# Kernel tuning notes

Measured on AMD Instinct MI355X. Metric: run time of the kernel, lower is better.

The kernel has to match this reference:

```python
import jax, jax.numpy as jnp
import numpy as np

EPS = 1e-5

def _layernorm(x, g, b):
    mu = jnp.mean(x, axis=-1, keepdims=True)
    var = jnp.mean(jnp.square(x - mu), axis=-1, keepdims=True)
    return (x - mu) * jax.lax.rsqrt(var + EPS) * g + b

def setup_inputs() -> dict:
    key = jax.random.key(0)
    ks = jax.random.split(key, 5)
    F_, H, D = 1024, 16, 64
    B, N = 4, 2048
    s = lambda k, shp, fan: jax.random.normal(k, shp, jnp.float32) * (fan ** -0.5)
    return {
        "x": jax.random.normal(ks[0], (B, N, F_), jnp.float32),
        "Wq": s(ks[1], (H * D, F_), F_),
        "Wkv": s(ks[2], (2 * H * D, F_), F_),
        "Wo": s(ks[3], (F_, H * D), H * D),
        "ln_g": jnp.ones((F_,), jnp.float32),
        "ln_b": jnp.zeros((F_,), jnp.float32),
        "lnc_g": jnp.ones((F_,), jnp.float32),
        "lnc_b": jnp.zeros((F_,), jnp.float32),
    }

def reference(x, Wq, Wkv, Wo, ln_g, ln_b, lnc_g, lnc_b):
    H, D = 16, 64
    scale = D ** -0.5
    skip = x
    xn = _layernorm(x, ln_g, ln_b)          # query path norm
    cn = _layernorm(x, lnc_g, lnc_b)        # context (self) norm
    B, N, _ = x.shape
    q = jnp.einsum('bnf,ef->bne', xn, Wq)   # [B,N,H*D]
    kv = jnp.einsum('bnf,ef->bne', cn, Wkv) # [B,N,2*H*D]
    k, v = jnp.split(kv, 2, axis=-1)
    tohd = lambda t: t.reshape(B, N, H, D).transpose(0, 2, 1, 3)  # b h n d
    q, k, v = tohd(q), tohd(k), tohd(v)
    sim = jnp.einsum('bhnd,bhmd->bhnm', q, k) * scale
    attn = jax.nn.softmax(sim, axis=-1)
    out = jnp.einsum('bhnm,bhmd->bhnd', attn, v)
    out = out.transpose(0, 2, 1, 3).reshape(B, N, H * D)
    out = jnp.einsum('bne,fe->bnf', out, Wo)
    return skip + out
```

## Files before the change

kernel.cpp:

```cpp
#include <hip/hip_runtime.h>
#include <hip/hip_bf16.h>
#include <stdint.h>

typedef __bf16 bf16;
typedef __bf16 bf16x8 __attribute__((ext_vector_type(8)));
typedef __bf16 bf16x4 __attribute__((ext_vector_type(4)));
typedef float f32x4 __attribute__((ext_vector_type(4)));
typedef unsigned u32x2 __attribute__((ext_vector_type(2)));

#define F_DIM 1024
#define NSEQ  2048
#define NB    4
#define NH    16
#define HD    64
#define MROWS (NB * NSEQ)
#define LOG2E 1.44269504088896340736f

__device__ __forceinline__ void gload_lds16(const void* g, void* l) {
    __builtin_amdgcn_global_load_lds(
        (__attribute__((address_space(1))) void*)g,
        (__attribute__((address_space(3))) void*)l,
        16, 0, 0);
}

__device__ __forceinline__ unsigned lds_addr(const void* p) {
    return (unsigned)(size_t)(__attribute__((address_space(3))) const void*)p;
}

__device__ __forceinline__ float exp2_fast(float x) {
    float r;
    asm("v_exp_f32 %0, %1" : "=v"(r) : "v"(x));
    return r;
}

__device__ __forceinline__ unsigned cvtpk_bf16(float lo, float hi) {
    unsigned r;
    asm("v_cvt_pk_bf16_f32 %0, %1, %2" : "=v"(r) : "v"(lo), "v"(hi));
    return r;
}

__global__ __launch_bounds__(256) void prep_kernel(
    const float* __restrict__ x,
    const float* __restrict__ g1, const float* __restrict__ b1,
    const float* __restrict__ g2, const float* __restrict__ b2,
    bf16* __restrict__ xn, bf16* __restrict__ cn,
    const float* __restrict__ wq, const float* __restrict__ wkv,
    const float* __restrict__ wo, bf16* __restrict__ wdst)
{
    const int t = threadIdx.x;
    if (blockIdx.x >= MROWS) {
        const int i = (blockIdx.x - MROWS) * 256 + t;
        const float* src;
        int si;
        if (i < 262144)       { src = wq;  si = i; }
        else if (i < 786432)  { src = wkv; si = i - 262144; }
        else                  { src = wo;  si = i - 786432; }
        float4 v = reinterpret_cast<const float4*>(src)[si];
        bf16x4 o = { (bf16)v.x, (bf16)v.y, (bf16)v.z, (bf16)v.w };
        reinterpret_cast<bf16x4*>(wdst)[i] = o;
        return;
    }
    const int row = blockIdx.x;
    float4 v = reinterpret_cast<const float4*>(x + (size_t)row * F_DIM)[t];
    float s  = v.x + v.y + v.z + v.w;
    float ss = v.x * v.x + v.y * v.y + v.z * v.z + v.w * v.w;
#pragma unroll
    for (int m = 1; m < 64; m <<= 1) {
        s  += __shfl_xor(s, m);
        ss += __shfl_xor(ss, m);
    }
    __shared__ float red[8];
    const int w = t >> 6;
    if ((t & 63) == 0) { red[w] = s; red[4 + w] = ss; }
    __syncthreads();
    s  = red[0] + red[1] + red[2] + red[3];
    ss = red[4] + red[5] + red[6] + red[7];
    const float mu  = s * (1.0f / F_DIM);
    const float var = fmaxf(ss * (1.0f / F_DIM) - mu * mu, 0.0f);
    const float rs  = rsqrtf(var + 1e-5f);

    float4 G1 = reinterpret_cast<const float4*>(g1)[t];
    float4 B1 = reinterpret_cast<const float4*>(b1)[t];
    float4 G2 = reinterpret_cast<const float4*>(g2)[t];
    float4 B2 = reinterpret_cast<const float4*>(b2)[t];
    const float h0 = (v.x - mu) * rs, h1 = (v.y - mu) * rs;
    const float h2 = (v.z - mu) * rs, h3 = (v.w - mu) * rs;
    bf16x4 o1 = { (bf16)(h0 * G1.x + B1.x), (bf16)(h1 * G1.y + B1.y),
                  (bf16)(h2 * G1.z + B1.z), (bf16)(h3 * G1.w + B1.w) };
    bf16x4 o2 = { (bf16)(h0 * G2.x + B2.x), (bf16)(h1 * G2.y + B2.y),
                  (bf16)(h2 * G2.z + B2.z), (bf16)(h3 * G2.w + B2.w) };
    *reinterpret_cast<bf16x4*>(xn + (size_t)row * F_DIM + t * 4) = o1;
    *reinterpret_cast<bf16x4*>(cn + (size_t)row * F_DIM + t * 4) = o2;
}

__global__ __launch_bounds__(256, 2) void qkv_gemm(
    const bf16* __restrict__ xn, const bf16* __restrict__ cn,
    const bf16* __restrict__ wq, const bf16* __restrict__ wkv,
    bf16* __restrict__ qb, bf16* __restrict__ kvb, float qscale)
{
    __shared__ bf16 As[128 * 32];
    __shared__ bf16 Bs[128 * 32];
    const int t = threadIdx.x;
    const int lane = t & 63;
    const int w = t >> 6;
    const int wr = w >> 1, wc = w & 1;

    int flat = blockIdx.x;
    flat = (flat & 7) * 192 + (flat >> 3);

    const bf16 *A, *B;
    bf16* C;
    int N, bm, bn;
    float osc;
    if (flat < 512) {
        A = xn; B = wq; C = qb; N = 1024; osc = qscale;
        bm = (flat >> 3) * 128; bn = (flat & 7) * 128;
    } else {
        const int f = flat - 512;
        A = cn; B = wkv; C = kvb; N = 2048; osc = 1.0f;
        bm = (f >> 4) * 128; bn = (f & 15) * 128;
    }

    const int r = lane & 15;
    const int kg = (lane >> 4) * 8;

    f32x4 acc[4][4];
#pragma unroll
    for (int i = 0; i < 4; i++)
#pragma unroll
        for (int j = 0; j < 4; j++) acc[i][j] = (f32x4){0.f, 0.f, 0.f, 0.f};

    const int c0 = t, c1 = 256 + t;
    const size_t aoff0 = (size_t)(bm + (c0 >> 2)) * F_DIM + (c0 & 3) * 8;
    const size_t aoff1 = (size_t)(bm + (c1 >> 2)) * F_DIM + (c1 & 3) * 8;
    const size_t boff0 = (size_t)(bn + (c0 >> 2)) * F_DIM + (c0 & 3) * 8;
    const size_t boff1 = (size_t)(bn + (c1 >> 2)) * F_DIM + (c1 & 3) * 8;
    bf16* lA0 = As + (size_t)(0 * 256 + w * 64) * 8;
    bf16* lA1 = As + (size_t)(1 * 256 + w * 64) * 8;
    bf16* lB0 = Bs + (size_t)(0 * 256 + w * 64) * 8;
    bf16* lB1 = Bs + (size_t)(1 * 256 + w * 64) * 8;

    for (int kt = 0; kt < F_DIM; kt += 32) {
        gload_lds16(A + aoff0 + kt, lA0);
        gload_lds16(A + aoff1 + kt, lA1);
        gload_lds16(B + boff0 + kt, lB0);
        gload_lds16(B + boff1 + kt, lB1);
        __syncthreads();
        bf16x8 af[4], bfr[4];
#pragma unroll
        for (int mi = 0; mi < 4; mi++)
            af[mi] = *(const bf16x8*)(As + (wr * 64 + mi * 16 + r) * 32 + kg);
#pragma unroll
        for (int ni = 0; ni < 4; ni++)
            bfr[ni] = *(const bf16x8*)(Bs + (wc * 64 + ni * 16 + r) * 32 + kg);
#pragma unroll
        for (int mi = 0; mi < 4; mi++)
#pragma unroll
            for (int ni = 0; ni < 4; ni++)
                acc[mi][ni] = __builtin_amdgcn_mfma_f32_16x16x32_bf16(
                    af[mi], bfr[ni], acc[mi][ni], 0, 0, 0);
        __syncthreads();
    }

    const int g = lane >> 4;
#pragma unroll
    for (int mi = 0; mi < 4; mi++) {
#pragma unroll
        for (int ni = 0; ni < 4; ni++) {
            const int col = bn + wc * 64 + ni * 16 + r;
#pragma unroll
            for (int j = 0; j < 4; j++) {
                const int row = bm + wr * 64 + mi * 16 + g * 4 + j;
                C[(size_t)row * N + col] = (bf16)(acc[mi][ni][j] * osc);
            }
        }
    }
}

__global__ __launch_bounds__(256, 2) void o_gemm(
    const bf16* __restrict__ A, const bf16* __restrict__ B,
    float* __restrict__ Cf, const float* __restrict__ skip)
{
    __shared__ bf16 As[128 * 32];
    __shared__ bf16 Bs[128 * 32];
    const int t = threadIdx.x;
    const int lane = t & 63;
    const int w = t >> 6;
    const int wr = w >> 1, wc = w & 1;

    int flat = blockIdx.x;
    flat = (flat & 7) * 64 + (flat >> 3);
    const int bm = (flat >> 3) * 128;
    const int bn = (flat & 7) * 128;

    const int r = lane & 15;
    const int kg = (lane >> 4) * 8;

    f32x4 acc[4][4];
#pragma unroll
    for (int i = 0; i < 4; i++)
#pragma unroll
        for (int j = 0; j < 4; j++) acc[i][j] = (f32x4){0.f, 0.f, 0.f, 0.f};

    const int c0 = t, c1 = 256 + t;
    const size_t aoff0 = (size_t)(bm + (c0 >> 2)) * F_DIM + (c0 & 3) * 8;
    const size_t aoff1 = (size_t)(bm + (c1 >> 2)) * F_DIM + (c1 & 3) * 8;
    const size_t boff0 = (size_t)(bn + (c0 >> 2)) * F_DIM + (c0 & 3) * 8;
    const size_t boff1 = (size_t)(bn + (c1 >> 2)) * F_DIM + (c1 & 3) * 8;
    bf16* lA0 = As + (size_t)(0 * 256 + w * 64) * 8;
    bf16* lA1 = As + (size_t)(1 * 256 + w * 64) * 8;
    bf16* lB0 = Bs + (size_t)(0 * 256 + w * 64) * 8;
    bf16* lB1 = Bs + (size_t)(1 * 256 + w * 64) * 8;

    for (int kt = 0; kt < F_DIM; kt += 32) {
        gload_lds16(A + aoff0 + kt, lA0);
        gload_lds16(A + aoff1 + kt, lA1);
        gload_lds16(B + boff0 + kt, lB0);
        gload_lds16(B + boff1 + kt, lB1);
        __syncthreads();
        bf16x8 af[4], bfr[4];
#pragma unroll
        for (int mi = 0; mi < 4; mi++)
            af[mi] = *(const bf16x8*)(As + (wr * 64 + mi * 16 + r) * 32 + kg);
#pragma unroll
        for (int ni = 0; ni < 4; ni++)
            bfr[ni] = *(const bf16x8*)(Bs + (wc * 64 + ni * 16 + r) * 32 + kg);
#pragma unroll
        for (int mi = 0; mi < 4; mi++)
#pragma unroll
            for (int ni = 0; ni < 4; ni++)
                acc[mi][ni] = __builtin_amdgcn_mfma_f32_16x16x32_bf16(
                    af[mi], bfr[ni], acc[mi][ni], 0, 0, 0);
        __syncthreads();
    }

    const int g = lane >> 4;
#pragma unroll
    for (int mi = 0; mi < 4; mi++) {
#pragma unroll
        for (int ni = 0; ni < 4; ni++) {
            const int col = bn + wc * 64 + ni * 16 + r;
#pragma unroll
            for (int j = 0; j < 4; j++) {
                const int row = bm + wr * 64 + mi * 16 + g * 4 + j;
                Cf[(size_t)row * F_DIM + col] =
                    acc[mi][ni][j] + skip[(size_t)row * F_DIM + col];
            }
        }
    }
}

__global__ __launch_bounds__(512)
__attribute__((amdgpu_waves_per_eu(4, 5)))
void attn_kernel(
    const bf16* __restrict__ q, const bf16* __restrict__ kvp,
    bf16* __restrict__ o)
{
    __shared__ __align__(16) bf16 Ks[128 * 64];
    __shared__ __align__(16) bf16 Vs[128 * 64];
    __shared__ __align__(16) bf16 Ps[8][16 * 72];

    const int bid = blockIdx.x;
    const int idx = (bid & 7) * 128 + (bid >> 3);
    const int bh = idx >> 4;
    const int qt = idx & 15;
    const int b = bh >> 4, h = bh & 15;

    const int t = threadIdx.x, lane = t & 63, w = t >> 6;
    const int r = lane & 15, g = lane >> 4;

    const size_t rowq = (size_t)b * NSEQ;

    size_t ksrc[2], vsrc[2];
#pragma unroll
    for (int c = 0; c < 2; c++) {
        const int p = c * 512 + t;
        const int krow = p >> 3;
        const int kcol = (p & 7) ^ (krow & 7);
        ksrc[c] = (size_t)(rowq + krow) * (2 * F_DIM) + h * HD + kcol * 8;
        const int kvb = p >> 5, dblk = (p >> 3) & 3;
        const int kvl = (p & 7) >> 1, d8 = p & 1;
        vsrc[c] = (size_t)(rowq + kvb * 4 + kvl) * (2 * F_DIM) + F_DIM + h * HD
                  + dblk * 16 + d8 * 8;
    }

    const int q0 = qt * 128 + w * 16;
    bf16x8 qf[2];
#pragma unroll
    for (int kk = 0; kk < 2; kk++)
        qf[kk] = *(const bf16x8*)(q + (rowq + q0 + r) * F_DIM + h * HD + kk * 32 + g * 8);

    f32x4 oacc[4];
#pragma unroll
    for (int i = 0; i < 4; i++) oacc[i] = (f32x4){0.f, 0.f, 0.f, 0.f};
    float m_r = -1e30f, l_r = 0.f;

    const unsigned va    = lds_addr(Vs) + (unsigned)(g * 1024 + r * 8);
    const unsigned pbase = lds_addr(&Ps[w][0]) + (unsigned)((r * 72 + g * 8) * 2);

    for (int kv0 = 0; kv0 < NSEQ; kv0 += 128) {
        asm volatile("s_barrier" ::: "memory");
        const size_t koff = (size_t)kv0 * (2 * F_DIM);
#pragma unroll
        for (int c = 0; c < 2; c++) {
            gload_lds16(kvp + ksrc[c] + koff, Ks + (size_t)(c * 512 + (t & ~63)) * 8);
            gload_lds16(kvp + vsrc[c] + koff, Vs + (size_t)(c * 512 + (t & ~63)) * 8);
        }
        asm volatile("s_waitcnt vmcnt(0)\n\ts_barrier" ::: "memory");

        f32x4 s4[8];
#pragma unroll
        for (int nt = 0; nt < 8; nt++) s4[nt] = (f32x4){0.f, 0.f, 0.f, 0.f};
        __builtin_amdgcn_s_setprio(1);
#pragma unroll
        for (int kk = 0; kk < 2; kk++) {
#pragma unroll
            for (int nt = 0; nt < 8; nt++) {
                const unsigned lb = (unsigned)((nt * 16 + r) * 128 + kk * 64 + g * 16)
                                    ^ (unsigned)((r & 7) << 4);
                bf16x8 kf = *(const bf16x8*)((const char*)Ks + lb);
                s4[nt] = __builtin_amdgcn_mfma_f32_16x16x32_bf16(kf, qf[kk], s4[nt], 0, 0, 0);
            }
        }
        __builtin_amdgcn_s_setprio(0);

        float mx = s4[0][0];
#pragma unroll
        for (int nt = 0; nt < 8; nt++)
#pragma unroll
            for (int j = 0; j < 4; j++) mx = fmaxf(mx, s4[nt][j]);
        mx = fmaxf(mx, __shfl_xor(mx, 16));
        mx = fmaxf(mx, __shfl_xor(mx, 32));
        if (!__all(mx <= m_r + 8.0f)) {
            const float mnew = fmaxf(m_r, mx);
            const float alpha = exp2_fast(m_r - mnew);
            l_r *= alpha;
#pragma unroll
            for (int j = 0; j < 4; j++) {
                const float aj = __shfl(alpha, g * 4 + j);
#pragma unroll
                for (int ntd = 0; ntd < 4; ntd++) oacc[ntd][j] *= aj;
            }
            m_r = mnew;
        }
        u32x2 pa2[8];
        float ps = 0.f;
#pragma unroll
        for (int nt = 0; nt < 8; nt++) {
            const float e0 = exp2_fast(s4[nt][0] - m_r);
            const float e1 = exp2_fast(s4[nt][1] - m_r);
            const float e2 = exp2_fast(s4[nt][2] - m_r);
            const float e3 = exp2_fast(s4[nt][3] - m_r);
            ps += (e0 + e1) + (e2 + e3);
            pa2[nt] = (u32x2){ cvtpk_bf16(e0, e1), cvtpk_bf16(e2, e3) };
        }
        ps += __shfl_xor(ps, 16);
        ps += __shfl_xor(ps, 32);
        l_r += ps;

#pragma unroll
        for (int hh = 0; hh < 2; hh++) {
#pragma unroll
            for (int nt2 = 0; nt2 < 4; nt2++)
                *(u32x2*)&Ps[w][r * 72 + nt2 * 16 + g * 4] = pa2[hh * 4 + nt2];
            asm volatile("s_waitcnt lgkmcnt(0)" ::: "memory");

            bf16x8 pf[2];
            u32x2 vt[2][4][2];
#pragma unroll
            for (int kk2 = 0; kk2 < 2; kk2++) {
                const unsigned pa = pbase + (unsigned)(kk2 * 64);
                asm volatile("ds_read_b128 %0, %1" : "=v"(pf[kk2]) : "v"(pa));
                const int kkg = hh * 2 + kk2;
#pragma unroll
                for (int ntd = 0; ntd < 4; ntd++) {
                    const unsigned a = va + (unsigned)(kkg * 4096 + ntd * 128);
                    asm volatile("ds_read_b64_tr_b16 %0, %2\n\t"
                                 "ds_read_b64_tr_b16 %1, %2 offset:512"
                                 : "=&v"(vt[kk2][ntd][0]), "=&v"(vt[kk2][ntd][1])
                                 : "v"(a));
                }
            }
            asm volatile("s_waitcnt lgkmcnt(0)" ::: "memory");
            __builtin_amdgcn_sched_barrier(0);

            __builtin_amdgcn_s_setprio(1);
#pragma unroll
            for (int kk2 = 0; kk2 < 2; kk2++)
#pragma unroll
                for (int ntd = 0; ntd < 4; ntd++) {
                    union { u32x2 hl[2]; bf16x8 v; } u;
                    u.hl[0] = vt[kk2][ntd][0];
                    u.hl[1] = vt[kk2][ntd][1];
                    oacc[ntd] = __builtin_amdgcn_mfma_f32_16x16x32_bf16(pf[kk2], u.v, oacc[ntd], 0, 0, 0);
                }
            __builtin_amdgcn_s_setprio(0);
        }
    }

    float rl[4];
#pragma unroll
    for (int j = 0; j < 4; j++) {
        const float lj = __shfl(l_r, g * 4 + j);
        rl[j] = 1.0f / lj;
    }
#pragma unroll
    for (int ntd = 0; ntd < 4; ntd++)
#pragma unroll
        for (int j = 0; j < 4; j++) {
            const int row = q0 + g * 4 + j;
            o[(rowq + row) * F_DIM + h * HD + ntd * 16 + r] =
                (bf16)(oacc[ntd][j] * rl[j]);
        }
}

extern "C" void kernel_launch(void* const* d_in, const int* in_sizes, int n_in,
                              void* d_out, int out_size, void* d_ws, size_t ws_size,
                              hipStream_t stream)
{
    const float* x     = (const float*)d_in[0];
    const float* Wq    = (const float*)d_in[1];
    const float* Wkv   = (const float*)d_in[2];
    const float* Wo    = (const float*)d_in[3];
    const float* ln_g  = (const float*)d_in[4];
    const float* ln_b  = (const float*)d_in[5];
    const float* lnc_g = (const float*)d_in[6];
    const float* lnc_b = (const float*)d_in[7];
    float* out = (float*)d_out;

    bf16* xn   = (bf16*)d_ws;
    bf16* cn   = xn  + (size_t)MROWS * F_DIM;
    bf16* qb   = cn  + (size_t)MROWS * F_DIM;
    bf16* kvb  = qb  + (size_t)MROWS * F_DIM;
    bf16* wqb  = kvb + (size_t)MROWS * 2 * F_DIM;
    bf16* wkvb = wqb + (size_t)F_DIM * F_DIM;
    bf16* wob  = wkvb + (size_t)2 * F_DIM * F_DIM;
    bf16* ao   = xn;

    prep_kernel<<<dim3(MROWS + 4096), dim3(256), 0, stream>>>(
        x, ln_g, ln_b, lnc_g, lnc_b, xn, cn, Wq, Wkv, Wo, wqb);

    qkv_gemm<<<dim3(1536), dim3(256), 0, stream>>>(
        xn, cn, wqb, wkvb, qb, kvb, 0.125f * LOG2E);
    attn_kernel<<<dim3(NSEQ / 128 * NB * NH), dim3(512), 0, stream>>>(qb, kvb, ao);
    o_gemm<<<dim3(512), dim3(256), 0, stream>>>(ao, wob, out, x);
}
```

Measured before the change: 215.5 us.

## Double-buffer K/V tiles in attention to overlap global loads with compute

Splits the 128-row K/V LDS tile into two 64-row ping-pong buffers and issues the asynchronous global-to-LDS load of the next 64-row tile before computing on the current one. This hides global memory latency behind the QK^T, softmax and PV work, where before every 128-row step stalled on vmcnt(0). The cost is twice as many barriers and online-softmax rescale checks per KV length, plus shorter MFMA bursts per tile. LDS usage stays the same.

```diff
diff --git a/kernel.cpp b/kernel.cpp
--- a/kernel.cpp
+++ b/kernel.cpp
@@ -256,8 +256,10 @@
     const bf16* __restrict__ q, const bf16* __restrict__ kvp,
     bf16* __restrict__ o)
 {
-    __shared__ __align__(16) bf16 Ks[128 * 64];
-    __shared__ __align__(16) bf16 Vs[128 * 64];
+    __shared__ __align__(16) bf16 Ks0[64 * 64];
+    __shared__ __align__(16) bf16 Ks1[64 * 64];
+    __shared__ __align__(16) bf16 Vs0[64 * 64];
+    __shared__ __align__(16) bf16 Vs1[64 * 64];
     __shared__ __align__(16) bf16 Ps[8][16 * 72];
 
     const int bid = blockIdx.x;
@@ -271,18 +273,17 @@
 
     const size_t rowq = (size_t)b * NSEQ;
 
-    size_t ksrc[2], vsrc[2];
-#pragma unroll
-    for (int c = 0; c < 2; c++) {
-        const int p = c * 512 + t;
-        const int krow = p >> 3;
-        const int kcol = (p & 7) ^ (krow & 7);
-        ksrc[c] = (size_t)(rowq + krow) * (2 * F_DIM) + h * HD + kcol * 8;
-        const int kvb = p >> 5, dblk = (p >> 3) & 3;
-        const int kvl = (p & 7) >> 1, d8 = p & 1;
-        vsrc[c] = (size_t)(rowq + kvb * 4 + kvl) * (2 * F_DIM) + F_DIM + h * HD
-                  + dblk * 16 + d8 * 8;
-    }
+    const int p = t;
+    const int krow = p >> 3;
+    const int kcol = (p & 7) ^ (krow & 7);
+    const size_t ksrc = (size_t)(rowq + krow) * (2 * F_DIM) + h * HD + kcol * 8;
+    const int kvb = p >> 5, dblk = (p >> 3) & 3;
+    const int kvl = (p & 7) >> 1, d8 = p & 1;
+    const size_t vsrc = (size_t)(rowq + kvb * 4 + kvl) * (2 * F_DIM) + F_DIM + h * HD
+                        + dblk * 16 + d8 * 8;
+    const unsigned wch = (unsigned)(t & ~63) * 8;
+    bf16* kd0 = Ks0 + wch;  bf16* kd1 = Ks1 + wch;
+    bf16* vd0 = Vs0 + wch;  bf16* vd1 = Vs1 + wch;
 
     const int q0 = qt * 128 + w * 16;
     bf16x8 qf[2];
@@ -295,108 +296,113 @@
     for (int i = 0; i < 4; i++) oacc[i] = (f32x4){0.f, 0.f, 0.f, 0.f};
     float m_r = -1e30f, l_r = 0.f;
 
-    const unsigned va    = lds_addr(Vs) + (unsigned)(g * 1024 + r * 8);
+    const unsigned va0   = lds_addr(Vs0) + (unsigned)(g * 1024 + r * 8);
+    const unsigned va1   = lds_addr(Vs1) + (unsigned)(g * 1024 + r * 8);
     const unsigned pbase = lds_addr(&Ps[w][0]) + (unsigned)((r * 72 + g * 8) * 2);
 
+    gload_lds16(kvp + ksrc, kd0);
+    gload_lds16(kvp + vsrc, vd0);
+
+#define ATTN_TILE(KSB, VAB, NKD, NVD, NOFF, MORE)                              \
+    {                                                                          \
+        asm volatile("s_waitcnt vmcnt(0)" ::: "memory");                       \
+        __builtin_amdgcn_s_barrier();                                          \
+        if (MORE) {                                                            \
+            gload_lds16(kvp + ksrc + (NOFF), NKD);                             \
+            gload_lds16(kvp + vsrc + (NOFF), NVD);                             \
+        }                                                                      \
+        f32x4 s4[4];                                                           \
+        _Pragma("unroll")                                                      \
+        for (int nt = 0; nt < 4; nt++) s4[nt] = (f32x4){0.f, 0.f, 0.f, 0.f};   \
+        __builtin_amdgcn_s_setprio(1);                                         \
+        _Pragma("unroll")                                                      \
+        for (int kk = 0; kk < 2; kk++) {                                       \
+            _Pragma("unroll")                                                  \
+            for (int nt = 0; nt < 4; nt++) {                                   \
+                const unsigned lb = (unsigned)((nt * 16 + r) * 128 + kk * 64   \
+                                    + g * 16) ^ (unsigned)((r & 7) << 4);      \
+                bf16x8 kf = *(const bf16x8*)((const char*)(KSB) + lb);         \
+                s4[nt] = __builtin_amdgcn_mfma_f32_16x16x32_bf16(              \
+                    kf, qf[kk], s4[nt], 0, 0, 0);                              \
+            }                                                                  \
+        }                                                                      \
+        __builtin_amdgcn_s_setprio(0);                                         \
+        float mx = s4[0][0];                                                   \
+        _Pragma("unroll")                                                      \
+        for (int nt = 0; nt < 4; nt++)                                         \
+            _Pragma("unroll")                                                  \
+            for (int j = 0; j < 4; j++) mx = fmaxf(mx, s4[nt][j]);             \
+        mx = fmaxf(mx, __shfl_xor(mx, 16));                                    \
+        mx = fmaxf(mx, __shfl_xor(mx, 32));                                    \
+        if (!__all(mx <= m_r + 8.0f)) {                                        \
+            const float mnew = fmaxf(m_r, mx);                                 \
+            const float alpha = exp2_fast(m_r - mnew);                         \
+            l_r *= alpha;                                                      \
+            _Pragma("unroll")                                                  \
+            for (int j = 0; j < 4; j++) {                                      \
+                const float aj = __shfl(alpha, g * 4 + j);                     \
+                _Pragma("unroll")                                              \
+                for (int ntd = 0; ntd < 4; ntd++) oacc[ntd][j] *= aj;          \
+            }                                                                  \
+            m_r = mnew;                                                        \
+        }                                                                      \
+        u32x2 pa2[4];                                                          \
+        float ps = 0.f;                                                        \
+        _Pragma("unroll")                                                      \
+        for (int nt = 0; nt < 4; nt++) {                                       \
+            const float e0 = exp2_fast(s4[nt][0] - m_r);                       \
+            const float e1 = exp2_fast(s4[nt][1] - m_r);                       \
+            const float e2 = exp2_fast(s4[nt][2] - m_r);                       \
+            const float e3 = exp2_fast(s4[nt][3] - m_r);                       \
+            ps += (e0 + e1) + (e2 + e3);                                       \
+            pa2[nt] = (u32x2){ cvtpk_bf16(e0, e1), cvtpk_bf16(e2, e3) };       \
+        }                                                                      \
+        ps += __shfl_xor(ps, 16);                                              \
+        ps += __shfl_xor(ps, 32);                                              \
+        l_r += ps;                                                             \
+        _Pragma("unroll")                                                      \
+        for (int nt = 0; nt < 4; nt++)                                         \
+            *(u32x2*)&Ps[w][r * 72 + nt * 16 + g * 4] = pa2[nt];               \
+        asm volatile("s_waitcnt lgkmcnt(0)" ::: "memory");                     \
+        bf16x8 pf[2];                                                          \
+        u32x2 vt[2][4][2];                                                     \
+        _Pragma("unroll")                                                      \
+        for (int kk2 = 0; kk2 < 2; kk2++) {                                    \
+            const unsigned pa = pbase + (unsigned)(kk2 * 64);                  \
+            asm volatile("ds_read_b128 %0, %1" : "=v"(pf[kk2]) : "v"(pa));     \
+            _Pragma("unroll")                                                  \
+            for (int ntd = 0; ntd < 4; ntd++) {                                \
+                const unsigned a = (VAB) + (unsigned)(kk2 * 4096 + ntd * 128); \
+                asm volatile("ds_read_b64_tr_b16 %0, %2\n\t"                   \
+                             "ds_read_b64_tr_b16 %1, %2 offset:512"            \
+                             : "=&v"(vt[kk2][ntd][0]), "=&v"(vt[kk2][ntd][1])  \
+                             : "v"(a));                                        \
+            }                                                                  \
+        }                                                                      \
+        asm volatile("s_waitcnt lgkmcnt(0)" ::: "memory");                     \
+        __builtin_amdgcn_sched_barrier(0);                                     \
+        __builtin_amdgcn_s_setprio(1);                                         \
+        _Pragma("unroll")                                                      \
+        for (int kk2 = 0; kk2 < 2; kk2++)                                      \
+            _Pragma("unroll")                                                  \
+            for (int ntd = 0; ntd < 4; ntd++) {                                \
+                union { u32x2 hl[2]; bf16x8 v; } u;                            \
+                u.hl[0] = vt[kk2][ntd][0];                                     \
+                u.hl[1] = vt[kk2][ntd][1];                                     \
+                oacc[ntd] = __builtin_amdgcn_mfma_f32_16x16x32_bf16(           \
+                    pf[kk2], u.v, oacc[ntd], 0, 0, 0);                         \
+            }                                                                  \
+        __builtin_amdgcn_s_setprio(0);                                         \
+    }
+
     for (int kv0 = 0; kv0 < NSEQ; kv0 += 128) {
-        asm volatile("s_barrier" ::: "memory");
-        const size_t koff = (size_t)kv0 * (2 * F_DIM);
-#pragma unroll
-        for (int c = 0; c < 2; c++) {
-            gload_lds16(kvp + ksrc[c] + koff, Ks + (size_t)(c * 512 + (t & ~63)) * 8);
-            gload_lds16(kvp + vsrc[c] + koff, Vs + (size_t)(c * 512 + (t & ~63)) * 8);
-        }
-        asm volatile("s_waitcnt vmcnt(0)\n\ts_barrier" ::: "memory");
-
-        f32x4 s4[8];
-#pragma unroll
-        for (int nt = 0; nt < 8; nt++) s4[nt] = (f32x4){0.f, 0.f, 0.f, 0.f};
-        __builtin_amdgcn_s_setprio(1);
-#pragma unroll
-        for (int kk = 0; kk < 2; kk++) {
-#pragma unroll
-            for (int nt = 0; nt < 8; nt++) {
-                const unsigned lb = (unsigned)((nt * 16 + r) * 128 + kk * 64 + g * 16)
-                                    ^ (unsigned)((r & 7) << 4);
-                bf16x8 kf = *(const bf16x8*)((const char*)Ks + lb);
-                s4[nt] = __builtin_amdgcn_mfma_f32_16x16x32_bf16(kf, qf[kk], s4[nt], 0, 0, 0);
-            }
-        }
-        __builtin_amdgcn_s_setprio(0);
-
-        float mx = s4[0][0];
-#pragma unroll
-        for (int nt = 0; nt < 8; nt++)
-#pragma unroll
-            for (int j = 0; j < 4; j++) mx = fmaxf(mx, s4[nt][j]);
-        mx = fmaxf(mx, __shfl_xor(mx, 16));
-        mx = fmaxf(mx, __shfl_xor(mx, 32));
-        if (!__all(mx <= m_r + 8.0f)) {
-            const float mnew = fmaxf(m_r, mx);
-            const float alpha = exp2_fast(m_r - mnew);
-            l_r *= alpha;
-#pragma unroll
-            for (int j = 0; j < 4; j++) {
-                const float aj = __shfl(alpha, g * 4 + j);
-#pragma unroll
-                for (int ntd = 0; ntd < 4; ntd++) oacc[ntd][j] *= aj;
-            }
-            m_r = mnew;
-        }
-        u32x2 pa2[8];
-        float ps = 0.f;
-#pragma unroll
-        for (int nt = 0; nt < 8; nt++) {
-            const float e0 = exp2_fast(s4[nt][0] - m_r);
-            const float e1 = exp2_fast(s4[nt][1] - m_r);
-            const float e2 = exp2_fast(s4[nt][2] - m_r);
-            const float e3 = exp2_fast(s4[nt][3] - m_r);
-            ps += (e0 + e1) + (e2 + e3);
-            pa2[nt] = (u32x2){ cvtpk_bf16(e0, e1), cvtpk_bf16(e2, e3) };
-        }
-        ps += __shfl_xor(ps, 16);
-        ps += __shfl_xor(ps, 32);
-        l_r += ps;
-
-#pragma unroll
-        for (int hh = 0; hh < 2; hh++) {
-#pragma unroll
-            for (int nt2 = 0; nt2 < 4; nt2++)
-                *(u32x2*)&Ps[w][r * 72 + nt2 * 16 + g * 4] = pa2[hh * 4 + nt2];
-            asm volatile("s_waitcnt lgkmcnt(0)" ::: "memory");
-
-            bf16x8 pf[2];
-            u32x2 vt[2][4][2];
-#pragma unroll
-            for (int kk2 = 0; kk2 < 2; kk2++) {
-                const unsigned pa = pbase + (unsigned)(kk2 * 64);
-                asm volatile("ds_read_b128 %0, %1" : "=v"(pf[kk2]) : "v"(pa));
-                const int kkg = hh * 2 + kk2;
-#pragma unroll
-                for (int ntd = 0; ntd < 4; ntd++) {
-                    const unsigned a = va + (unsigned)(kkg * 4096 + ntd * 128);
-                    asm volatile("ds_read_b64_tr_b16 %0, %2\n\t"
-                                 "ds_read_b64_tr_b16 %1, %2 offset:512"
-                                 : "=&v"(vt[kk2][ntd][0]), "=&v"(vt[kk2][ntd][1])
-                                 : "v"(a));
-                }
-            }
-            asm volatile("s_waitcnt lgkmcnt(0)" ::: "memory");
-            __builtin_amdgcn_sched_barrier(0);
-
-            __builtin_amdgcn_s_setprio(1);
-#pragma unroll
-            for (int kk2 = 0; kk2 < 2; kk2++)
-#pragma unroll
-                for (int ntd = 0; ntd < 4; ntd++) {
-                    union { u32x2 hl[2]; bf16x8 v; } u;
-                    u.hl[0] = vt[kk2][ntd][0];
-                    u.hl[1] = vt[kk2][ntd][1];
-                    oacc[ntd] = __builtin_amdgcn_mfma_f32_16x16x32_bf16(pf[kk2], u.v, oacc[ntd], 0, 0, 0);
-                }
-            __builtin_amdgcn_s_setprio(0);
-        }
-    }
+        const size_t offB = (size_t)(kv0 + 64) * (2 * F_DIM);
+        const size_t offA = (size_t)(kv0 + 128) * (2 * F_DIM);
+        const bool moreA = (kv0 + 128 < NSEQ);
+        ATTN_TILE(Ks0, va0, kd1, vd1, offB, true);
+        ATTN_TILE(Ks1, va1, kd0, vd0, offA, moreA);
+    }
+#undef ATTN_TILE
 
     float rl[4];
 #pragma unroll
```

Result: no change. 217.6 us (+1.0%).
